# Kernel tuning notes

Measured on AMD Instinct MI355X. Metric: run time of the kernel, lower is better.

The kernel has to match this reference:

```python
import jax, jax.numpy as jnp
import numpy as np

QMAX = 7.0   # int4 symmetric, narrow range [-7, 7] per weight; acts use [-8, 7]
QMIN = -8.0

def _ste_quant(v, scale, qmin, qmax):
    """Symmetric per-tensor fake-quant with straight-through estimator."""
    s = jax.lax.stop_gradient(scale)
    q = jnp.clip(jnp.round(v / s), qmin, qmax) * s
    return v + jax.lax.stop_gradient(q - v)


def setup_inputs() -> dict:
    key = jax.random.key(0)
    k1, k2, k3 = jax.random.split(key, 3)
    d_model, vocab = 1024, 50257
    x = jax.random.normal(k1, (2, 1024, d_model), jnp.float32)
    W = jax.random.normal(k2, (vocab, d_model), jnp.float32) * 0.02
    b = jax.random.normal(k3, (vocab,), jnp.float32) * 0.01
    return {"x": x, "W": W, "b": b}


def reference(x, W, b):
    # Activation quant: 4-bit signed, per-tensor scale from max-abs stats
    sx = jnp.max(jnp.abs(x)) / QMAX
    xq = _ste_quant(x, sx, QMIN, QMAX)
    # Weight quant: 4-bit signed per-tensor
    sw = jnp.max(jnp.abs(W)) / QMAX
    wq = _ste_quant(W, sw, QMIN, QMAX)
    # Int32 bias: quantized at the accumulator scale sx*sw (range huge -> round only)
    sb = jax.lax.stop_gradient(sx * sw)
    bq = b + jax.lax.stop_gradient(jnp.round(b / sb) * sb - b)
    # Quantized GEMM with int32-style accumulation, expressed as dequantized matmul
    logits = jnp.einsum('bsd,vd->bsv', xq, wq) + bq  # [B, S, vocab]
    return jax.nn.log_softmax(logits, axis=-1)
```

## Files before the change

### kernel.cpp

```cpp
#include <hip/hip_runtime.h>
#include <hip/hip_bf16.h>

#define N_VOCAB 50257
#define NB      393
#define N_PAD   50304
#define D_K     1024
#define M_ROWS  2048
#define GEMM_BLOCKS (NB * 16)
#define PER_XCD     (GEMM_BLOCKS/8)

typedef __attribute__((ext_vector_type(4))) int i32x4;

__device__ inline void async_copy16(const void* g, void* l) {
  auto* gp = (const __attribute__((address_space(1))) unsigned int*)g;
  auto* lp = (__attribute__((address_space(3))) unsigned int*)l;
  __builtin_amdgcn_global_load_lds(gp, lp, 16, 0, 0);
}

__device__ inline signed char qint(float v, float s) {
  float q = fminf(fmaxf(rintf(v / s), -8.f), 7.f);
  return (signed char)(int)q;
}

__global__ void absmax2_kernel(const float4* __restrict__ x, int nx4,
                               const float4* __restrict__ Wp, int nw4,
                               unsigned* __restrict__ amax) {
  const bool isx = blockIdx.x < 512;
  const float4* p = isx ? x : Wp;
  const int n4 = isx ? nx4 : nw4;
  const int b0 = isx ? blockIdx.x : blockIdx.x - 512;
  const int nb = isx ? 512 : (gridDim.x - 512);
  float m = 0.f;
  for (int i = b0 * blockDim.x + threadIdx.x; i < n4; i += nb * blockDim.x) {
    float4 v = p[i];
    m = fmaxf(m, fmaxf(fmaxf(fabsf(v.x), fabsf(v.y)),
                       fmaxf(fabsf(v.z), fabsf(v.w))));
  }
#pragma unroll
  for (int off = 32; off; off >>= 1) m = fmaxf(m, __shfl_xor(m, off));
  __shared__ float red[4];
  int tid = threadIdx.x;
  if ((tid & 63) == 0) red[tid >> 6] = m;
  __syncthreads();
  if (tid == 0) {
    m = fmaxf(fmaxf(red[0], red[1]), fmaxf(red[2], red[3]));
    atomicMax(&amax[isx ? 0 : 1], __float_as_uint(m));
  }
}

__global__ void quant_kernel(const float4* __restrict__ x,
                             const float4* __restrict__ Wp,
                             const float* __restrict__ b,
                             char4* __restrict__ qx, char4* __restrict__ qw,
                             float* __restrict__ bq,
                             const unsigned* __restrict__ amax) {
  const int bid = blockIdx.x;
  const int tid = threadIdx.x;
  const int nw4 = (N_VOCAB * D_K) / 4;
  if (bid < 2048) {
    int i = bid * 256 + tid;
    float s = __uint_as_float(amax[0]) * (1.0f / 7.0f);
    float4 v = x[i];
    char4 q;
    q.x = qint(v.x, s); q.y = qint(v.y, s);
    q.z = qint(v.z, s); q.w = qint(v.w, s);
    qx[i] = q;
  } else if (bid < 2048 + 50304) {
    int i = (bid - 2048) * 256 + tid;
    char4 q = {0, 0, 0, 0};
    if (i < nw4) {
      float s = __uint_as_float(amax[1]) * (1.0f / 7.0f);
      float4 v = Wp[i];
      q.x = qint(v.x, s); q.y = qint(v.y, s);
      q.z = qint(v.z, s); q.w = qint(v.w, s);
    }
    qw[i] = q;
  } else {
    int i = (bid - (2048 + 50304)) * 256 + tid;
    if (i < N_PAD) {
      float v = 0.f;
      if (i < N_VOCAB) {
        float sb = (__uint_as_float(amax[0]) * (1.0f / 7.0f)) *
                   (__uint_as_float(amax[1]) * (1.0f / 7.0f));
        v = rintf(b[i] / sb) * sb;
      }
      bq[i] = v;
    }
  }
}

__global__ __launch_bounds__(256, 3) void gemm_kernel(
    const signed char* __restrict__ qx,
    const signed char* __restrict__ qw,
    const float* __restrict__ bq,
    const unsigned* __restrict__ amax,
    float* __restrict__ outp,
    float* __restrict__ pmax,
    float* __restrict__ psum)
{
  constexpr int BK = 64;
  constexpr int NT = D_K / BK;
  __shared__ __align__(16) signed char sA[3][128 * BK];
  __shared__ __align__(16) signed char sB[3][128 * BK];
  __shared__ float redMax[128][2];
  __shared__ float redSum[128][2];

  const int tid = threadIdx.x;
  const int l = tid & 63;
  const int w = tid >> 6;
  const int wr = w >> 1, wc = w & 1;

  const int bid = blockIdx.x;
  const int vb = (bid & 7) * PER_XCD + (bid >> 3);
  const int nb = vb >> 4;
  const int m0 = (vb & 15) * 128;
  const int n0 = nb * 128;

  const float sx = __uint_as_float(amax[0]) * (1.0f / 7.0f);
  const float sw = __uint_as_float(amax[1]) * (1.0f / 7.0f);
  const float scale = sx * sw;

  i32x4 acc[4][4] = {};

  const int srow = (l >> 2);
  const int scol = ((l & 3) ^ ((l >> 3) & 3)) * 16;

  auto stage = [&](int buf, int kt) {
    int k0 = kt * BK;
#pragma unroll
    for (int i = 0; i < 2; ++i) {
      int c = w * 2 + i;
      int row = c * 16 + srow;
      async_copy16(qx + (size_t)(m0 + row) * D_K + k0 + scol,
                   &sA[buf][c * 1024]);
      async_copy16(qw + (size_t)(n0 + row) * D_K + k0 + scol,
                   &sB[buf][c * 1024]);
    }
  };

  stage(0, 0);
  stage(1, 1);
  asm volatile("s_waitcnt vmcnt(4)" ::: "memory");
  __builtin_amdgcn_s_barrier();
  __builtin_amdgcn_sched_barrier(0);

#pragma unroll
  for (int kt = 0; kt < NT; ++kt) {
    const int cur = kt % 3;

    i32x4 af[4], bfr[4];
#pragma unroll
    for (int mi = 0; mi < 4; ++mi) {
      int row = wr * 64 + mi * 16 + (l & 15);
      int kb = ((l >> 4) ^ ((row >> 1) & 3)) * 16;
      af[mi] = *(const i32x4*)&sA[cur][row * BK + kb];
    }
#pragma unroll
    for (int ni = 0; ni < 4; ++ni) {
      int row = wc * 64 + ni * 16 + (l & 15);
      int kb = ((l >> 4) ^ ((row >> 1) & 3)) * 16;
      bfr[ni] = *(const i32x4*)&sB[cur][row * BK + kb];
    }

    if (kt + 2 < NT) stage((kt + 2) % 3, kt + 2);

    __builtin_amdgcn_s_setprio(1);
#pragma unroll
    for (int mi = 0; mi < 4; ++mi)
#pragma unroll
      for (int ni = 0; ni < 4; ++ni)
        acc[mi][ni] = __builtin_amdgcn_mfma_i32_16x16x64_i8(
            af[mi], bfr[ni], acc[mi][ni], 0, 0, 0);
    __builtin_amdgcn_s_setprio(0);
    __builtin_amdgcn_sched_barrier(0);

    if (kt + 1 < NT) {
      if (kt + 2 < NT)
        asm volatile("s_waitcnt vmcnt(4)" ::: "memory");
      else
        asm volatile("s_waitcnt vmcnt(0)" ::: "memory");
      __builtin_amdgcn_s_barrier();
      __builtin_amdgcn_sched_barrier(0);
    }
  }

  bool valid[4];
  float bb[4];
#pragma unroll
  for (int ni = 0; ni < 4; ++ni) {
    int col = n0 + wc * 64 + ni * 16 + (l & 15);
    valid[ni] = (col < N_VOCAB);
    bb[ni] = valid[ni] ? bq[col] : 0.f;
  }
  float lg[4][4][4];
#pragma unroll
  for (int mi = 0; mi < 4; ++mi)
#pragma unroll
    for (int ni = 0; ni < 4; ++ni)
#pragma unroll
      for (int r = 0; r < 4; ++r)
        lg[mi][ni][r] = (float)acc[mi][ni][r] * scale + bb[ni];

  float rmax[4][4];
#pragma unroll
  for (int mi = 0; mi < 4; ++mi)
#pragma unroll
    for (int r = 0; r < 4; ++r) {
      float mval = -3.4e38f;
#pragma unroll
      for (int ni = 0; ni < 4; ++ni)
        if (valid[ni]) mval = fmaxf(mval, lg[mi][ni][r]);
#pragma unroll
      for (int off = 1; off < 16; off <<= 1)
        mval = fmaxf(mval, __shfl_xor(mval, off));
      rmax[mi][r] = mval;
      if ((l & 15) == 0)
        redMax[wr * 64 + mi * 16 + (l >> 4) * 4 + r][wc] = mval;
    }
  __syncthreads();

#pragma unroll
  for (int mi = 0; mi < 4; ++mi)
#pragma unroll
    for (int r = 0; r < 4; ++r) {
      int rl = wr * 64 + mi * 16 + (l >> 4) * 4 + r;
      float gmax = fmaxf(redMax[rl][0], redMax[rl][1]);
      float s = 0.f;
#pragma unroll
      for (int ni = 0; ni < 4; ++ni)
        if (valid[ni]) s += __expf(lg[mi][ni][r] - gmax);
#pragma unroll
      for (int off = 1; off < 16; off <<= 1)
        s += __shfl_xor(s, off);
      if ((l & 15) == 0) redSum[rl][wc] = s;
      rmax[mi][r] = gmax;
    }
  __syncthreads();

  if (wc == 0 && (l & 15) == 0) {
#pragma unroll
    for (int mi = 0; mi < 4; ++mi)
#pragma unroll
      for (int r = 0; r < 4; ++r) {
        int rl = wr * 64 + mi * 16 + (l >> 4) * 4 + r;
        int rowg = m0 + rl;
        pmax[(size_t)rowg * NB + nb] = rmax[mi][r];
        psum[(size_t)rowg * NB + nb] = redSum[rl][0] + redSum[rl][1];
      }
  }

#pragma unroll
  for (int mi = 0; mi < 4; ++mi)
#pragma unroll
    for (int r = 0; r < 4; ++r) {
      int rowg = m0 + wr * 64 + mi * 16 + (l >> 4) * 4 + r;
      size_t rb = (size_t)rowg * N_VOCAB;
#pragma unroll
      for (int ni = 0; ni < 4; ++ni) {
        if (valid[ni]) {
          int col = n0 + wc * 64 + ni * 16 + (l & 15);
          outp[rb + col] = lg[mi][ni][r];
        }
      }
    }
}

__global__ __launch_bounds__(256) void finalize_kernel(
    const float* __restrict__ pmax, const float* __restrict__ psum,
    float* __restrict__ logz) {
  const int row = blockIdx.x;
  const float* pm = pmax + (size_t)row * NB;
  const float* ps = psum + (size_t)row * NB;
  const int tid = threadIdx.x;
  __shared__ float red[8];

  float m = -3.4e38f;
  for (int i = tid; i < NB; i += 256) m = fmaxf(m, pm[i]);
#pragma unroll
  for (int off = 32; off; off >>= 1) m = fmaxf(m, __shfl_xor(m, off));
  if ((tid & 63) == 0) red[tid >> 6] = m;
  __syncthreads();
  m = fmaxf(fmaxf(red[0], red[1]), fmaxf(red[2], red[3]));

  float s = 0.f;
  for (int i = tid; i < NB; i += 256) s += ps[i] * __expf(pm[i] - m);
#pragma unroll
  for (int off = 32; off; off >>= 1) s += __shfl_xor(s, off);
  if ((tid & 63) == 0) red[4 + (tid >> 6)] = s;
  __syncthreads();
  if (tid == 0) {
    s = red[4] + red[5] + red[6] + red[7];
    logz[row] = m + __logf(s);
  }
}

__global__ __launch_bounds__(256) void subtract_kernel(
    float* __restrict__ out, const float* __restrict__ logz) {
  const int row = blockIdx.x;
  const float lz = logz[row];
  const size_t base = (size_t)row * N_VOCAB;
  const int tid = threadIdx.x;
  const int a = (4 - (row & 3)) & 3;
  if (tid < a) out[base + tid] -= lz;
  const int n4 = (N_VOCAB - a) >> 2;
  float4* p = (float4*)(out + base + a);
  for (int i = tid; i < n4; i += 256) {
    float4 v = p[i];
    v.x -= lz; v.y -= lz; v.z -= lz; v.w -= lz;
    p[i] = v;
  }
  const int done = a + n4 * 4;
  if (tid < N_VOCAB - done) out[base + done + tid] -= lz;
}

extern "C" void kernel_launch(void* const* d_in, const int* in_sizes, int n_in,
                              void* d_out, int out_size, void* d_ws,
                              size_t ws_size, hipStream_t stream) {
  const float* x = (const float*)d_in[0];
  const float* W = (const float*)d_in[1];
  const float* b = (const float*)d_in[2];
  float* out = (float*)d_out;

  char* ws = (char*)d_ws;
  unsigned* amax = (unsigned*)ws;
  float* bq = (float*)(ws + 4096);
  float* logz = (float*)(ws + (1ull << 20));
  float* pmax = (float*)(ws + (2ull << 20));
  float* psum = (float*)(ws + (6ull << 20));
  signed char* qx = (signed char*)(ws + (10ull << 20));
  signed char* qw = (signed char*)(ws + (14ull << 20));

  hipMemsetAsync(amax, 0, 8, stream);

  const int nx4 = (M_ROWS * D_K) / 4;
  const int nw4 = (N_VOCAB * D_K) / 4;

  absmax2_kernel<<<2560, 256, 0, stream>>>((const float4*)x, nx4,
                                           (const float4*)W, nw4, amax);

  quant_kernel<<<2048 + 50304 + 197, 256, 0, stream>>>(
      (const float4*)x, (const float4*)W, b, (char4*)qx, (char4*)qw, bq, amax);

  gemm_kernel<<<GEMM_BLOCKS, 256, 0, stream>>>(qx, qw, bq, amax, out, pmax,
                                               psum);

  finalize_kernel<<<M_ROWS, 256, 0, stream>>>(pmax, psum, logz);

  subtract_kernel<<<M_ROWS, 256, 0, stream>>>(out, logz);
}
```

Before: 577.4 us.

## Use 256x128 GEMM tiles with 512-thread blocks and double-buffered LDS

Each GEMM block now has 8 waves and covers 256 rows instead of 128, so every staged weight tile is reused across twice as many activation rows and the block count halves. The LDS pipeline goes from three stages with hand-placed vmcnt waits to two-stage double buffering with a __syncthreads each iteration, and the softmax reduction scratch now reuses the A-tile buffer. This cuts weight-side global traffic per output but leaves less load/compute overlap, adds heavier barriers, and the launch bound of 6 blocks of 512 threads may limit registers.

```diff
diff --git a/kernel.cpp b/kernel.cpp
--- a/kernel.cpp
+++ b/kernel.cpp
@@ -6,7 +6,7 @@
 #define N_PAD   50304
 #define D_K     1024
 #define M_ROWS  2048
-#define GEMM_BLOCKS (NB * 16)
+#define GEMM_BLOCKS (NB * 8)
 #define PER_XCD     (GEMM_BLOCKS/8)
 
 typedef __attribute__((ext_vector_type(4))) int i32x4;
@@ -89,7 +89,7 @@
   }
 }
 
-__global__ __launch_bounds__(256, 3) void gemm_kernel(
+__global__ __launch_bounds__(512, 6) void gemm_kernel(
     const signed char* __restrict__ qx,
     const signed char* __restrict__ qw,
     const float* __restrict__ bq,
@@ -100,20 +100,19 @@
 {
   constexpr int BK = 64;
   constexpr int NT = D_K / BK;
-  __shared__ __align__(16) signed char sA[3][128 * BK];
-  __shared__ __align__(16) signed char sB[3][128 * BK];
-  __shared__ float redMax[128][2];
-  __shared__ float redSum[128][2];
+  __shared__ __align__(16) signed char sA[2][256 * BK];
+  __shared__ __align__(16) signed char sB[2][128 * BK];
 
   const int tid = threadIdx.x;
   const int l = tid & 63;
   const int w = tid >> 6;
-  const int wr = w >> 1, wc = w & 1;
+  const int wr = w >> 1;
+  const int wc = w & 1;
 
   const int bid = blockIdx.x;
   const int vb = (bid & 7) * PER_XCD + (bid >> 3);
-  const int nb = vb >> 4;
-  const int m0 = (vb & 15) * 128;
+  const int nb = vb >> 3;
+  const int m0 = (vb & 7) * 256;
   const int n0 = nb * 128;
 
   const float sx = __uint_as_float(amax[0]) * (1.0f / 7.0f);
@@ -122,7 +121,7 @@
 
   i32x4 acc[4][4] = {};
 
-  const int srow = (l >> 2);
+  const int srow = l >> 2;
   const int scol = ((l & 3) ^ ((l >> 3) & 3)) * 16;
 
   auto stage = [&](int buf, int kt) {
@@ -133,20 +132,21 @@
       int row = c * 16 + srow;
       async_copy16(qx + (size_t)(m0 + row) * D_K + k0 + scol,
                    &sA[buf][c * 1024]);
+    }
+    {
+      int c = w;
+      int row = c * 16 + srow;
       async_copy16(qw + (size_t)(n0 + row) * D_K + k0 + scol,
                    &sB[buf][c * 1024]);
     }
   };
 
   stage(0, 0);
-  stage(1, 1);
-  asm volatile("s_waitcnt vmcnt(4)" ::: "memory");
-  __builtin_amdgcn_s_barrier();
-  __builtin_amdgcn_sched_barrier(0);
-
-#pragma unroll
+  __syncthreads();
+
+  int cur = 0;
   for (int kt = 0; kt < NT; ++kt) {
-    const int cur = kt % 3;
+    if (kt + 1 < NT) stage(cur ^ 1, kt + 1);
 
     i32x4 af[4], bfr[4];
 #pragma unroll
@@ -162,8 +162,6 @@
       bfr[ni] = *(const i32x4*)&sB[cur][row * BK + kb];
     }
 
-    if (kt + 2 < NT) stage((kt + 2) % 3, kt + 2);
-
     __builtin_amdgcn_s_setprio(1);
 #pragma unroll
     for (int mi = 0; mi < 4; ++mi)
@@ -172,16 +170,9 @@
         acc[mi][ni] = __builtin_amdgcn_mfma_i32_16x16x64_i8(
             af[mi], bfr[ni], acc[mi][ni], 0, 0, 0);
     __builtin_amdgcn_s_setprio(0);
-    __builtin_amdgcn_sched_barrier(0);
-
-    if (kt + 1 < NT) {
-      if (kt + 2 < NT)
-        asm volatile("s_waitcnt vmcnt(4)" ::: "memory");
-      else
-        asm volatile("s_waitcnt vmcnt(0)" ::: "memory");
-      __builtin_amdgcn_s_barrier();
-      __builtin_amdgcn_sched_barrier(0);
-    }
+
+    __syncthreads();
+    cur ^= 1;
   }
 
   bool valid[4];
@@ -201,6 +192,9 @@
       for (int r = 0; r < 4; ++r)
         lg[mi][ni][r] = (float)acc[mi][ni][r] * scale + bb[ni];
 
+  float* redMax = (float*)&sA[0][0];
+  float* redSum = redMax + 512;
+
   float rmax[4][4];
 #pragma unroll
   for (int mi = 0; mi < 4; ++mi)
@@ -215,7 +209,7 @@
         mval = fmaxf(mval, __shfl_xor(mval, off));
       rmax[mi][r] = mval;
       if ((l & 15) == 0)
-        redMax[wr * 64 + mi * 16 + (l >> 4) * 4 + r][wc] = mval;
+        redMax[(wr * 64 + mi * 16 + (l >> 4) * 4 + r) * 2 + wc] = mval;
     }
   __syncthreads();
 
@@ -224,7 +218,7 @@
 #pragma unroll
     for (int r = 0; r < 4; ++r) {
       int rl = wr * 64 + mi * 16 + (l >> 4) * 4 + r;
-      float gmax = fmaxf(redMax[rl][0], redMax[rl][1]);
+      float gmax = fmaxf(redMax[rl * 2 + 0], redMax[rl * 2 + 1]);
       float s = 0.f;
 #pragma unroll
       for (int ni = 0; ni < 4; ++ni)
@@ -232,7 +226,7 @@
 #pragma unroll
       for (int off = 1; off < 16; off <<= 1)
         s += __shfl_xor(s, off);
-      if ((l & 15) == 0) redSum[rl][wc] = s;
+      if ((l & 15) == 0) redSum[rl * 2 + wc] = s;
       rmax[mi][r] = gmax;
     }
   __syncthreads();
@@ -245,7 +239,7 @@
         int rl = wr * 64 + mi * 16 + (l >> 4) * 4 + r;
         int rowg = m0 + rl;
         pmax[(size_t)rowg * NB + nb] = rmax[mi][r];
-        psum[(size_t)rowg * NB + nb] = redSum[rl][0] + redSum[rl][1];
+        psum[(size_t)rowg * NB + nb] = redSum[rl * 2 + 0] + redSum[rl * 2 + 1];
       }
   }
 
@@ -341,7 +335,7 @@
   quant_kernel<<<2048 + 50304 + 197, 256, 0, stream>>>(
       (const float4*)x, (const float4*)W, b, (char4*)qx, (char4*)qw, bq, amax);
 
-  gemm_kernel<<<GEMM_BLOCKS, 256, 0, stream>>>(qx, qw, bq, amax, out, pmax,
+  gemm_kernel<<<GEMM_BLOCKS, 512, 0, stream>>>(qx, qw, bq, amax, out, pmax,
                                                psum);
 
   finalize_kernel<<<M_ROWS, 256, 0, stream>>>(pmax, psum, logz);
```

Result: slower. 1.584 ms (+174.3%).

## Double-buffer A tile, reuse LDS for reductions, fuse logZ with subtract

Applied to the files above, without the earlier changes.

Stages the activation tile with two LDS buffers while keeping three for weights, and reuses the weight buffer for softmax reduction scratch. This shrinks per-block LDS so the GEMM can target four blocks per CU. It also merges the finalize and subtract kernels into one launch that computes logZ in shared memory. The cost is a shorter prefetch distance for A, which may expose load latency, plus an extra barrier before the reduction.

```diff
diff --git a/kernel.cpp b/kernel.cpp
--- a/kernel.cpp
+++ b/kernel.cpp
@@ -89,7 +89,7 @@
   }
 }
 
-__global__ __launch_bounds__(256, 3) void gemm_kernel(
+__global__ __launch_bounds__(256, 4) void gemm_kernel(
     const signed char* __restrict__ qx,
     const signed char* __restrict__ qw,
     const float* __restrict__ bq,
@@ -100,10 +100,8 @@
 {
   constexpr int BK = 64;
   constexpr int NT = D_K / BK;
-  __shared__ __align__(16) signed char sA[3][128 * BK];
+  __shared__ __align__(16) signed char sA[2][128 * BK];
   __shared__ __align__(16) signed char sB[3][128 * BK];
-  __shared__ float redMax[128][2];
-  __shared__ float redSum[128][2];
 
   const int tid = threadIdx.x;
   const int l = tid & 63;
@@ -122,10 +120,10 @@
 
   i32x4 acc[4][4] = {};
 
-  const int srow = (l >> 2);
+  const int srow = l >> 2;
   const int scol = ((l & 3) ^ ((l >> 3) & 3)) * 16;
 
-  auto stage = [&](int buf, int kt) {
+  auto stageA = [&](int buf, int kt) {
     int k0 = kt * BK;
 #pragma unroll
     for (int i = 0; i < 2; ++i) {
@@ -133,36 +131,47 @@
       int row = c * 16 + srow;
       async_copy16(qx + (size_t)(m0 + row) * D_K + k0 + scol,
                    &sA[buf][c * 1024]);
+    }
+  };
+  auto stageB = [&](int buf, int kt) {
+    int k0 = kt * BK;
+#pragma unroll
+    for (int i = 0; i < 2; ++i) {
+      int c = w * 2 + i;
+      int row = c * 16 + srow;
       async_copy16(qw + (size_t)(n0 + row) * D_K + k0 + scol,
                    &sB[buf][c * 1024]);
     }
   };
 
-  stage(0, 0);
-  stage(1, 1);
-  asm volatile("s_waitcnt vmcnt(4)" ::: "memory");
+  stageA(0, 0);
+  stageB(0, 0);
+  stageB(1, 1);
+  asm volatile("s_waitcnt vmcnt(2)" ::: "memory");
   __builtin_amdgcn_s_barrier();
   __builtin_amdgcn_sched_barrier(0);
 
 #pragma unroll
   for (int kt = 0; kt < NT; ++kt) {
-    const int cur = kt % 3;
+    const int ca = kt & 1;
+    const int cb = kt % 3;
 
     i32x4 af[4], bfr[4];
 #pragma unroll
     for (int mi = 0; mi < 4; ++mi) {
       int row = wr * 64 + mi * 16 + (l & 15);
       int kb = ((l >> 4) ^ ((row >> 1) & 3)) * 16;
-      af[mi] = *(const i32x4*)&sA[cur][row * BK + kb];
+      af[mi] = *(const i32x4*)&sA[ca][row * BK + kb];
     }
 #pragma unroll
     for (int ni = 0; ni < 4; ++ni) {
       int row = wc * 64 + ni * 16 + (l & 15);
       int kb = ((l >> 4) ^ ((row >> 1) & 3)) * 16;
-      bfr[ni] = *(const i32x4*)&sB[cur][row * BK + kb];
-    }
-
-    if (kt + 2 < NT) stage((kt + 2) % 3, kt + 2);
+      bfr[ni] = *(const i32x4*)&sB[cb][row * BK + kb];
+    }
+
+    if (kt + 1 < NT) stageA(ca ^ 1, kt + 1);
+    if (kt + 2 < NT) stageB((kt + 2) % 3, kt + 2);
 
     __builtin_amdgcn_s_setprio(1);
 #pragma unroll
@@ -176,7 +185,7 @@
 
     if (kt + 1 < NT) {
       if (kt + 2 < NT)
-        asm volatile("s_waitcnt vmcnt(4)" ::: "memory");
+        asm volatile("s_waitcnt vmcnt(2)" ::: "memory");
       else
         asm volatile("s_waitcnt vmcnt(0)" ::: "memory");
       __builtin_amdgcn_s_barrier();
@@ -201,6 +210,10 @@
       for (int r = 0; r < 4; ++r)
         lg[mi][ni][r] = (float)acc[mi][ni][r] * scale + bb[ni];
 
+  __syncthreads();
+  float* redMax = (float*)&sB[0][0];
+  float* redSum = redMax + 256;
+
   float rmax[4][4];
 #pragma unroll
   for (int mi = 0; mi < 4; ++mi)
@@ -215,7 +228,7 @@
         mval = fmaxf(mval, __shfl_xor(mval, off));
       rmax[mi][r] = mval;
       if ((l & 15) == 0)
-        redMax[wr * 64 + mi * 16 + (l >> 4) * 4 + r][wc] = mval;
+        redMax[(wr * 64 + mi * 16 + (l >> 4) * 4 + r) * 2 + wc] = mval;
     }
   __syncthreads();
 
@@ -224,7 +237,7 @@
 #pragma unroll
     for (int r = 0; r < 4; ++r) {
       int rl = wr * 64 + mi * 16 + (l >> 4) * 4 + r;
-      float gmax = fmaxf(redMax[rl][0], redMax[rl][1]);
+      float gmax = fmaxf(redMax[rl * 2 + 0], redMax[rl * 2 + 1]);
       float s = 0.f;
 #pragma unroll
       for (int ni = 0; ni < 4; ++ni)
@@ -232,7 +245,7 @@
 #pragma unroll
       for (int off = 1; off < 16; off <<= 1)
         s += __shfl_xor(s, off);
-      if ((l & 15) == 0) redSum[rl][wc] = s;
+      if ((l & 15) == 0) redSum[rl * 2 + wc] = s;
       rmax[mi][r] = gmax;
     }
   __syncthreads();
@@ -245,7 +258,7 @@
         int rl = wr * 64 + mi * 16 + (l >> 4) * 4 + r;
         int rowg = m0 + rl;
         pmax[(size_t)rowg * NB + nb] = rmax[mi][r];
-        psum[(size_t)rowg * NB + nb] = redSum[rl][0] + redSum[rl][1];
+        psum[(size_t)rowg * NB + nb] = redSum[rl * 2 + 0] + redSum[rl * 2 + 1];
       }
   }
 
@@ -265,14 +278,14 @@
     }
 }
 
-__global__ __launch_bounds__(256) void finalize_kernel(
+__global__ __launch_bounds__(256) void logz_sub_kernel(
     const float* __restrict__ pmax, const float* __restrict__ psum,
-    float* __restrict__ logz) {
+    float* __restrict__ out) {
   const int row = blockIdx.x;
   const float* pm = pmax + (size_t)row * NB;
   const float* ps = psum + (size_t)row * NB;
   const int tid = threadIdx.x;
-  __shared__ float red[8];
+  __shared__ float red[9];
 
   float m = -3.4e38f;
   for (int i = tid; i < NB; i += 256) m = fmaxf(m, pm[i]);
@@ -290,16 +303,12 @@
   __syncthreads();
   if (tid == 0) {
     s = red[4] + red[5] + red[6] + red[7];
-    logz[row] = m + __logf(s);
-  }
-}
-
-__global__ __launch_bounds__(256) void subtract_kernel(
-    float* __restrict__ out, const float* __restrict__ logz) {
-  const int row = blockIdx.x;
-  const float lz = logz[row];
+    red[8] = m + __logf(s);
+  }
+  __syncthreads();
+  const float lz = red[8];
+
   const size_t base = (size_t)row * N_VOCAB;
-  const int tid = threadIdx.x;
   const int a = (4 - (row & 3)) & 3;
   if (tid < a) out[base + tid] -= lz;
   const int n4 = (N_VOCAB - a) >> 2;
@@ -324,7 +333,6 @@
   char* ws = (char*)d_ws;
   unsigned* amax = (unsigned*)ws;
   float* bq = (float*)(ws + 4096);
-  float* logz = (float*)(ws + (1ull << 20));
   float* pmax = (float*)(ws + (2ull << 20));
   float* psum = (float*)(ws + (6ull << 20));
   signed char* qx = (signed char*)(ws + (10ull << 20));
@@ -344,7 +352,5 @@
   gemm_kernel<<<GEMM_BLOCKS, 256, 0, stream>>>(qx, qw, bq, amax, out, pmax,
                                                psum);
 
-  finalize_kernel<<<M_ROWS, 256, 0, stream>>>(pmax, psum, logz);
-
-  subtract_kernel<<<M_ROWS, 256, 0, stream>>>(out, logz);
-}
+  logz_sub_kernel<<<M_ROWS, 256, 0, stream>>>(pmax, psum, out);
+}
```

Measured after the change: 553.3 us. 1.04x faster.

## Use single-wave 64x64 GEMM tiles and fuse logZ finalize with subtract

Applied to the files above, without the earlier changes.

The GEMM changes from 256-thread 128x128 tiles with a 3-stage LDS pipeline to 64-thread single-wave 64x64 tiles with double buffering. This removes block barriers and the cross-wave LDS reduction for row max and sum. The finalize and subtract kernels merge into one kernel that uses two blocks per row and drops one launch and the logz round trip. In exchange each block gets half the data reuse, global load traffic per MFMA doubles, and the partial max/sum arrays double in size.

```diff
diff --git a/kernel.cpp b/kernel.cpp
--- a/kernel.cpp
+++ b/kernel.cpp
@@ -2,11 +2,12 @@
 #include <hip/hip_bf16.h>
 
 #define N_VOCAB 50257
-#define NB      393
+#define NBC     786
 #define N_PAD   50304
 #define D_K     1024
 #define M_ROWS  2048
-#define GEMM_BLOCKS (NB * 16)
+#define MT      32
+#define GEMM_BLOCKS (NBC * MT)
 #define PER_XCD     (GEMM_BLOCKS/8)
 
 typedef __attribute__((ext_vector_type(4))) int i32x4;
@@ -89,7 +90,7 @@
   }
 }
 
-__global__ __launch_bounds__(256, 3) void gemm_kernel(
+__global__ __launch_bounds__(64, 2) void gemm_kernel(
     const signed char* __restrict__ qx,
     const signed char* __restrict__ qw,
     const float* __restrict__ bq,
@@ -100,21 +101,16 @@
 {
   constexpr int BK = 64;
   constexpr int NT = D_K / BK;
-  __shared__ __align__(16) signed char sA[3][128 * BK];
-  __shared__ __align__(16) signed char sB[3][128 * BK];
-  __shared__ float redMax[128][2];
-  __shared__ float redSum[128][2];
-
-  const int tid = threadIdx.x;
-  const int l = tid & 63;
-  const int w = tid >> 6;
-  const int wr = w >> 1, wc = w & 1;
+  __shared__ __align__(16) signed char sA[2][64 * BK];
+  __shared__ __align__(16) signed char sB[2][64 * BK];
+
+  const int l = threadIdx.x & 63;
 
   const int bid = blockIdx.x;
   const int vb = (bid & 7) * PER_XCD + (bid >> 3);
-  const int nb = vb >> 4;
-  const int m0 = (vb & 15) * 128;
-  const int n0 = nb * 128;
+  const int nb = vb >> 5;
+  const int m0 = (vb & 31) * 64;
+  const int n0 = nb * 64;
 
   const float sx = __uint_as_float(amax[0]) * (1.0f / 7.0f);
   const float sw = __uint_as_float(amax[1]) * (1.0f / 7.0f);
@@ -122,17 +118,20 @@
 
   i32x4 acc[4][4] = {};
 
-  const int srow = (l >> 2);
+  const int srow = l >> 2;
   const int scol = ((l & 3) ^ ((l >> 3) & 3)) * 16;
 
   auto stage = [&](int buf, int kt) {
     int k0 = kt * BK;
 #pragma unroll
-    for (int i = 0; i < 2; ++i) {
-      int c = w * 2 + i;
+    for (int c = 0; c < 4; ++c) {
       int row = c * 16 + srow;
       async_copy16(qx + (size_t)(m0 + row) * D_K + k0 + scol,
                    &sA[buf][c * 1024]);
+    }
+#pragma unroll
+    for (int c = 0; c < 4; ++c) {
+      int row = c * 16 + srow;
       async_copy16(qw + (size_t)(n0 + row) * D_K + k0 + scol,
                    &sB[buf][c * 1024]);
     }
@@ -140,55 +139,49 @@
 
   stage(0, 0);
   stage(1, 1);
-  asm volatile("s_waitcnt vmcnt(4)" ::: "memory");
-  __builtin_amdgcn_s_barrier();
-  __builtin_amdgcn_sched_barrier(0);
 
 #pragma unroll
   for (int kt = 0; kt < NT; ++kt) {
-    const int cur = kt % 3;
+    const int cur = kt & 1;
+
+    if (kt + 1 < NT)
+      asm volatile("s_waitcnt vmcnt(8)" ::: "memory");
+    else
+      asm volatile("s_waitcnt vmcnt(0)" ::: "memory");
+    __builtin_amdgcn_sched_barrier(0);
 
     i32x4 af[4], bfr[4];
 #pragma unroll
     for (int mi = 0; mi < 4; ++mi) {
-      int row = wr * 64 + mi * 16 + (l & 15);
+      int row = mi * 16 + (l & 15);
       int kb = ((l >> 4) ^ ((row >> 1) & 3)) * 16;
       af[mi] = *(const i32x4*)&sA[cur][row * BK + kb];
     }
 #pragma unroll
     for (int ni = 0; ni < 4; ++ni) {
-      int row = wc * 64 + ni * 16 + (l & 15);
+      int row = ni * 16 + (l & 15);
       int kb = ((l >> 4) ^ ((row >> 1) & 3)) * 16;
       bfr[ni] = *(const i32x4*)&sB[cur][row * BK + kb];
     }
-
-    if (kt + 2 < NT) stage((kt + 2) % 3, kt + 2);
-
-    __builtin_amdgcn_s_setprio(1);
+    asm volatile("s_waitcnt lgkmcnt(0)" ::: "memory");
+    __builtin_amdgcn_sched_barrier(0);
+
+    if (kt + 2 < NT) stage(cur, kt + 2);
+    __builtin_amdgcn_sched_barrier(0);
+
 #pragma unroll
     for (int mi = 0; mi < 4; ++mi)
 #pragma unroll
       for (int ni = 0; ni < 4; ++ni)
         acc[mi][ni] = __builtin_amdgcn_mfma_i32_16x16x64_i8(
             af[mi], bfr[ni], acc[mi][ni], 0, 0, 0);
-    __builtin_amdgcn_s_setprio(0);
-    __builtin_amdgcn_sched_barrier(0);
-
-    if (kt + 1 < NT) {
-      if (kt + 2 < NT)
-        asm volatile("s_waitcnt vmcnt(4)" ::: "memory");
-      else
-        asm volatile("s_waitcnt vmcnt(0)" ::: "memory");
-      __builtin_amdgcn_s_barrier();
-      __builtin_amdgcn_sched_barrier(0);
-    }
   }
 
   bool valid[4];
   float bb[4];
 #pragma unroll
   for (int ni = 0; ni < 4; ++ni) {
-    int col = n0 + wc * 64 + ni * 16 + (l & 15);
+    int col = n0 + ni * 16 + (l & 15);
     valid[ni] = (col < N_VOCAB);
     bb[ni] = valid[ni] ? bq[col] : 0.f;
   }
@@ -201,7 +194,6 @@
       for (int r = 0; r < 4; ++r)
         lg[mi][ni][r] = (float)acc[mi][ni][r] * scale + bb[ni];
 
-  float rmax[4][4];
 #pragma unroll
   for (int mi = 0; mi < 4; ++mi)
 #pragma unroll
@@ -213,69 +205,48 @@
 #pragma unroll
       for (int off = 1; off < 16; off <<= 1)
         mval = fmaxf(mval, __shfl_xor(mval, off));
-      rmax[mi][r] = mval;
-      if ((l & 15) == 0)
-        redMax[wr * 64 + mi * 16 + (l >> 4) * 4 + r][wc] = mval;
-    }
-  __syncthreads();
-
-#pragma unroll
-  for (int mi = 0; mi < 4; ++mi)
-#pragma unroll
-    for (int r = 0; r < 4; ++r) {
-      int rl = wr * 64 + mi * 16 + (l >> 4) * 4 + r;
-      float gmax = fmaxf(redMax[rl][0], redMax[rl][1]);
       float s = 0.f;
 #pragma unroll
       for (int ni = 0; ni < 4; ++ni)
-        if (valid[ni]) s += __expf(lg[mi][ni][r] - gmax);
+        if (valid[ni]) s += __expf(lg[mi][ni][r] - mval);
 #pragma unroll
       for (int off = 1; off < 16; off <<= 1)
         s += __shfl_xor(s, off);
-      if ((l & 15) == 0) redSum[rl][wc] = s;
-      rmax[mi][r] = gmax;
-    }
-  __syncthreads();
-
-  if (wc == 0 && (l & 15) == 0) {
-#pragma unroll
-    for (int mi = 0; mi < 4; ++mi)
-#pragma unroll
-      for (int r = 0; r < 4; ++r) {
-        int rl = wr * 64 + mi * 16 + (l >> 4) * 4 + r;
-        int rowg = m0 + rl;
-        pmax[(size_t)rowg * NB + nb] = rmax[mi][r];
-        psum[(size_t)rowg * NB + nb] = redSum[rl][0] + redSum[rl][1];
+      if ((l & 15) == 0) {
+        int rowg = m0 + mi * 16 + (l >> 4) * 4 + r;
+        pmax[(size_t)rowg * NBC + nb] = mval;
+        psum[(size_t)rowg * NBC + nb] = s;
       }
-  }
+    }
 
 #pragma unroll
   for (int mi = 0; mi < 4; ++mi)
 #pragma unroll
     for (int r = 0; r < 4; ++r) {
-      int rowg = m0 + wr * 64 + mi * 16 + (l >> 4) * 4 + r;
+      int rowg = m0 + mi * 16 + (l >> 4) * 4 + r;
       size_t rb = (size_t)rowg * N_VOCAB;
 #pragma unroll
       for (int ni = 0; ni < 4; ++ni) {
         if (valid[ni]) {
-          int col = n0 + wc * 64 + ni * 16 + (l & 15);
+          int col = n0 + ni * 16 + (l & 15);
           outp[rb + col] = lg[mi][ni][r];
         }
       }
     }
 }
 
-__global__ __launch_bounds__(256) void finalize_kernel(
+__global__ __launch_bounds__(256) void logz_sub_kernel(
     const float* __restrict__ pmax, const float* __restrict__ psum,
-    float* __restrict__ logz) {
-  const int row = blockIdx.x;
-  const float* pm = pmax + (size_t)row * NB;
-  const float* ps = psum + (size_t)row * NB;
+    float* __restrict__ out) {
+  const int row = blockIdx.x >> 1;
+  const int half = blockIdx.x & 1;
+  const float* pm = pmax + (size_t)row * NBC;
+  const float* ps = psum + (size_t)row * NBC;
   const int tid = threadIdx.x;
-  __shared__ float red[8];
+  __shared__ float red[9];
 
   float m = -3.4e38f;
-  for (int i = tid; i < NB; i += 256) m = fmaxf(m, pm[i]);
+  for (int i = tid; i < NBC; i += 256) m = fmaxf(m, pm[i]);
 #pragma unroll
   for (int off = 32; off; off >>= 1) m = fmaxf(m, __shfl_xor(m, off));
   if ((tid & 63) == 0) red[tid >> 6] = m;
@@ -283,34 +254,36 @@
   m = fmaxf(fmaxf(red[0], red[1]), fmaxf(red[2], red[3]));
 
   float s = 0.f;
-  for (int i = tid; i < NB; i += 256) s += ps[i] * __expf(pm[i] - m);
+  for (int i = tid; i < NBC; i += 256) s += ps[i] * __expf(pm[i] - m);
 #pragma unroll
   for (int off = 32; off; off >>= 1) s += __shfl_xor(s, off);
   if ((tid & 63) == 0) red[4 + (tid >> 6)] = s;
   __syncthreads();
   if (tid == 0) {
     s = red[4] + red[5] + red[6] + red[7];
-    logz[row] = m + __logf(s);
-  }
-}
-
-__global__ __launch_bounds__(256) void subtract_kernel(
-    float* __restrict__ out, const float* __restrict__ logz) {
-  const int row = blockIdx.x;
-  const float lz = logz[row];
+    red[8] = m + __logf(s);
+  }
+  __syncthreads();
+  const float lz = red[8];
+
   const size_t base = (size_t)row * N_VOCAB;
-  const int tid = threadIdx.x;
   const int a = (4 - (row & 3)) & 3;
-  if (tid < a) out[base + tid] -= lz;
   const int n4 = (N_VOCAB - a) >> 2;
+  const int h4 = (n4 + 1) >> 1;
+  const int i0 = half * h4;
+  const int i1 = min(n4, i0 + h4);
   float4* p = (float4*)(out + base + a);
-  for (int i = tid; i < n4; i += 256) {
+  for (int i = i0 + tid; i < i1; i += 256) {
     float4 v = p[i];
     v.x -= lz; v.y -= lz; v.z -= lz; v.w -= lz;
     p[i] = v;
   }
-  const int done = a + n4 * 4;
-  if (tid < N_VOCAB - done) out[base + done + tid] -= lz;
+  if (half == 0) {
+    if (tid < a) out[base + tid] -= lz;
+  } else {
+    const int done = a + n4 * 4;
+    if (tid < N_VOCAB - done) out[base + done + tid] -= lz;
+  }
 }
 
 extern "C" void kernel_launch(void* const* d_in, const int* in_sizes, int n_in,
@@ -324,11 +297,10 @@
   char* ws = (char*)d_ws;
   unsigned* amax = (unsigned*)ws;
   float* bq = (float*)(ws + 4096);
-  float* logz = (float*)(ws + (1ull << 20));
-  float* pmax = (float*)(ws + (2ull << 20));
-  float* psum = (float*)(ws + (6ull << 20));
-  signed char* qx = (signed char*)(ws + (10ull << 20));
-  signed char* qw = (signed char*)(ws + (14ull << 20));
+  float* pmax = (float*)(ws + (1ull << 20));
+  float* psum = (float*)(ws + (8ull << 20));
+  signed char* qx = (signed char*)(ws + (15ull << 20));
+  signed char* qw = (signed char*)(ws + (17ull << 20));
 
   hipMemsetAsync(amax, 0, 8, stream);
 
@@ -341,10 +313,8 @@
   quant_kernel<<<2048 + 50304 + 197, 256, 0, stream>>>(
       (const float4*)x, (const float4*)W, b, (char4*)qx, (char4*)qw, bq, amax);
 
-  gemm_kernel<<<GEMM_BLOCKS, 256, 0, stream>>>(qx, qw, bq, amax, out, pmax,
-                                               psum);
-
-  finalize_kernel<<<M_ROWS, 256, 0, stream>>>(pmax, psum, logz);
-
-  subtract_kernel<<<M_ROWS, 256, 0, stream>>>(out, logz);
-}
+  gemm_kernel<<<GEMM_BLOCKS, 64, 0, stream>>>(qx, qw, bq, amax, out, pmax,
+                                              psum);
+
+  logz_sub_kernel<<<M_ROWS * 2, 256, 0, stream>>>(pmax, psum, out);
+}
```

Result: slower. 631.9 us (+9.4%).
